# Optimization experiments

Measured on AMD Instinct MI355X. Metric: run time of the kernel, lower is better.

The kernel has to match this reference:

```python
import jax, jax.numpy as jnp
import numpy as np

N_EMB = 512
E_DIM = 64
COMMIT_COST = 0.25


def setup_inputs() -> dict:
    key = jax.random.key(0)
    k1, k2 = jax.random.split(key)
    z = jax.random.normal(k1, (32, E_DIM, 64, 64), dtype=jnp.float32)  # [B,C,H,W], C==e_dim
    # nn.Embedding weight init: uniform(-1/n_emb, 1/n_emb)
    emb_weight = jax.random.uniform(k2, (N_EMB, E_DIM), dtype=jnp.float32,
                                    minval=-1.0 / N_EMB, maxval=1.0 / N_EMB)
    return {"z": z, "emb_weight": emb_weight}


def reference(z, emb_weight):
    sg = jax.lax.stop_gradient
    B, C, H, W = z.shape
    zp = jnp.transpose(z, (0, 2, 3, 1))            # [B,H,W,C]
    zf = zp.reshape(-1, C)                          # [N,C]
    # pairwise squared distances: ||z||^2 + ||e||^2 - 2 z e^T  -> [N, n_emb]
    d = (jnp.sum(zf * zf, axis=1, keepdims=True)
         + jnp.sum(emb_weight * emb_weight, axis=1)
         - 2.0 * jnp.matmul(zf, emb_weight.T))
    idx = jnp.argmin(d, axis=1)                     # [N]
    min_encodings = jax.nn.one_hot(idx, N_EMB, dtype=z.dtype)  # [N, n_emb]
    # one-hot @ weight == direct gather
    z_q = jnp.take(emb_weight, idx, axis=0).reshape(zp.shape)  # [B,H,W,C]
    loss = (jnp.mean((sg(z_q) - zp) ** 2)
            + COMMIT_COST * jnp.mean((z_q - sg(zp)) ** 2))
    z_q = zp + sg(z_q - zp)                         # straight-through
    e_mean = jnp.mean(min_encodings, axis=0)
    perplexity = jnp.exp(-jnp.sum(e_mean * jnp.log(e_mean + 1e-10)))
    z_q = jnp.transpose(z_q, (0, 3, 1, 2))          # back to [B,C,H,W]
    return (loss, z_q, perplexity, min_encodings, idx[:, None])
```

## Files before the change

### kernel.cpp

```cpp
#include <hip/hip_runtime.h>
#include <math.h>

#define OUT_ZQ   1LL
#define OUT_PERP 8388609LL
#define OUT_ENC  8388610LL
#define OUT_IDX  75497474LL

#define WS_HIST   0
#define WS_LOSS64 512
#define WS_ESUM   1024
#define WS_PK     4096
#define LOSS_SCALE 16777216.0

typedef __attribute__((ext_vector_type(8))) short bf16x8;
typedef __attribute__((ext_vector_type(4))) float f32x4;

__device__ __forceinline__ unsigned short f2bf(float f) {
  unsigned u = __builtin_bit_cast(unsigned, f);
  u += 0x7FFFu + ((u >> 16) & 1u);
  return (unsigned short)(u >> 16);
}

__global__ void vq_prep(const float* __restrict__ E, float* __restrict__ ws) {
#pragma clang fp contract(off)
  const int T   = blockIdx.x;
  const int tid = threadIdx.x;
  const int l   = tid & 63;
  const int kk  = tid >> 6;
  const int g = l >> 4, ln16 = l & 15;
  {
    const float* ej = E + (size_t)(T * 16 + ln16) * 64;
    const int c0 = kk * 32 + 4 * g;
    bf16x8 v;
#pragma unroll
    for (int i = 0; i < 4; ++i) v[i]     = (short)f2bf(ej[c0 + i]);
#pragma unroll
    for (int i = 0; i < 4; ++i) v[4 + i] = (short)f2bf(ej[c0 + 16 + i]);
    ((bf16x8*)(ws + WS_PK))[(T * 2 + kk) * 64 + l] = v;
  }
  if (tid < 16) {
    const int j = T * 16 + tid;
    const float* e = E + (size_t)j * 64;
    float q0=e[0]*e[0],q1=e[1]*e[1],q2=e[2]*e[2],q3=e[3]*e[3];
    float q4=e[4]*e[4],q5=e[5]*e[5],q6=e[6]*e[6],q7=e[7]*e[7];
#pragma unroll
    for (int i = 8; i < 64; i += 8) {
      q0+=e[i+0]*e[i+0]; q1+=e[i+1]*e[i+1]; q2+=e[i+2]*e[i+2]; q3+=e[i+3]*e[i+3];
      q4+=e[i+4]*e[i+4]; q5+=e[i+5]*e[i+5]; q6+=e[i+6]*e[i+6]; q7+=e[i+7]*e[i+7];
    }
    ws[WS_ESUM + j] = ((q0+q1)+(q2+q3))+((q4+q5)+(q6+q7));
  }
  if (T == 0) {
#pragma unroll
    for (int k = 0; k < 4; ++k) ((int*)ws)[WS_HIST + tid + k * 128] = 0;
    if (tid == 0) *((unsigned long long*)(ws + WS_LOSS64)) = 0ull;
  }
}

__global__ __launch_bounds__(256, 4) void vq_main(const float* __restrict__ z,
                                                  const float* __restrict__ E,
                                                  float* __restrict__ ws,
                                                  float* __restrict__ out) {
#pragma clang fp contract(off)
  const int tid  = threadIdx.x;
  const int lane = tid & 63;
  const int wv   = __builtin_amdgcn_readfirstlane(tid >> 6);
  const int g    = lane >> 4;
  const int ln16 = lane & 15;
  const int row  = blockIdx.x;
  const int b = row >> 6, h = row & 63;
  const size_t zbase = (size_t)b * 262144 + (size_t)h * 64;
  const float* __restrict__ esg = ws + WS_ESUM;
  const bf16x8* __restrict__ pkt = (const bf16x8*)(ws + WS_PK);
  float4* __restrict__ enc4 = (float4*)(out + OUT_ENC + (size_t)row * 32768);
  const float4 zz4 = {0.f, 0.f, 0.f, 0.f};
#define FILLC(cc) _Pragma("unroll") \
  for (int fi = (cc)*8; fi < (cc)*8 + 8; ++fi) enc4[(size_t)fi * 256 + tid] = zz4;

  __shared__ float lds_z[64][65];
  __shared__ float s_zsum[64];
  __shared__ float s_qpart[4][64];
  __shared__ float s_qthr[64];
  __shared__ int   s_cnt[64];
  __shared__ int   s_ovf[64];
  __shared__ int   s_idx[64];
  __shared__ int   s_cand[64][12];
  __shared__ float s_dcand[64][12];
  __shared__ float s_l[4];

#pragma unroll
  for (int k = 0; k < 16; ++k) {
    int c = k * 4 + wv;
    lds_z[lane][c] = z[zbase + (size_t)c * 4096 + lane];
  }
  if (tid < 64) { s_cnt[tid] = 0; s_ovf[tid] = 0; }
  FILLC(0)
  __syncthreads();

  if (tid < 64) {
    const float* zl = &lds_z[tid][0];
    float q0=zl[0]*zl[0],q1=zl[1]*zl[1],q2=zl[2]*zl[2],q3=zl[3]*zl[3];
    float q4=zl[4]*zl[4],q5=zl[5]*zl[5],q6=zl[6]*zl[6],q7=zl[7]*zl[7];
#pragma unroll
    for (int i = 8; i < 64; i += 8) {
      q0+=zl[i+0]*zl[i+0]; q1+=zl[i+1]*zl[i+1]; q2+=zl[i+2]*zl[i+2]; q3+=zl[i+3]*zl[i+3];
      q4+=zl[i+4]*zl[i+4]; q5+=zl[i+5]*zl[i+5]; q6+=zl[i+6]*zl[i+6]; q7+=zl[i+7]*zl[i+7];
    }
    s_zsum[tid] = ((q0+q1)+(q2+q3))+((q4+q5)+(q6+q7));
  }

  bf16x8 Af[4][2];
#pragma unroll
  for (int mt = 0; mt < 4; ++mt) {
    int m = mt * 16 + ln16;
#pragma unroll
    for (int kk = 0; kk < 2; ++kk) {
      int c0 = kk * 32 + 4 * g;
      bf16x8 v;
#pragma unroll
      for (int i = 0; i < 4; ++i) v[i]     = (short)f2bf(lds_z[m][c0 + i]);
#pragma unroll
      for (int i = 0; i < 4; ++i) v[4 + i] = (short)f2bf(lds_z[m][c0 + 16 + i]);
      Af[mt][kk] = v;
    }
  }

  float qmin[4][4];
#pragma unroll
  for (int mt = 0; mt < 4; ++mt)
#pragma unroll
    for (int r = 0; r < 4; ++r) qmin[mt][r] = 1e30f;
#pragma unroll
  for (int t = 0; t < 8; ++t) {
    const int T = wv * 8 + t;
    const int j = T * 16 + ln16;
    bf16x8 B0 = pkt[(T * 2 + 0) * 64 + lane];
    bf16x8 B1 = pkt[(T * 2 + 1) * 64 + lane];
    float es = esg[j];
#pragma unroll
    for (int mt = 0; mt < 4; ++mt) {
      f32x4 C = {0.f, 0.f, 0.f, 0.f};
      C = __builtin_amdgcn_mfma_f32_16x16x32_bf16(Af[mt][0], B0, C, 0, 0, 0);
      C = __builtin_amdgcn_mfma_f32_16x16x32_bf16(Af[mt][1], B1, C, 0, 0, 0);
#pragma unroll
      for (int r = 0; r < 4; ++r)
        qmin[mt][r] = fminf(qmin[mt][r], es - 2.0f * C[r]);
    }
  }
#pragma unroll
  for (int off = 1; off < 16; off <<= 1)
#pragma unroll
    for (int mt = 0; mt < 4; ++mt)
#pragma unroll
      for (int r = 0; r < 4; ++r)
        qmin[mt][r] = fminf(qmin[mt][r], __shfl_xor(qmin[mt][r], off));
  if (ln16 == 0)
#pragma unroll
    for (int mt = 0; mt < 4; ++mt)
#pragma unroll
      for (int r = 0; r < 4; ++r)
        s_qpart[wv][mt * 16 + g * 4 + r] = qmin[mt][r];
  FILLC(1)
  __syncthreads();
  if (tid < 64) {
    float qm = fminf(fminf(s_qpart[0][tid], s_qpart[1][tid]),
                     fminf(s_qpart[2][tid], s_qpart[3][tid]));
    s_qthr[tid] = qm + (2.5e-4f * sqrtf(s_zsum[tid]) + 1e-4f);
  }
  __syncthreads();

#pragma unroll
  for (int t = 0; t < 8; ++t) {
    const int T = wv * 8 + t;
    const int j = T * 16 + ln16;
    bf16x8 B0 = pkt[(T * 2 + 0) * 64 + lane];
    bf16x8 B1 = pkt[(T * 2 + 1) * 64 + lane];
    float es = esg[j];
#pragma unroll
    for (int mt = 0; mt < 4; ++mt) {
      f32x4 C = {0.f, 0.f, 0.f, 0.f};
      C = __builtin_amdgcn_mfma_f32_16x16x32_bf16(Af[mt][0], B0, C, 0, 0, 0);
      C = __builtin_amdgcn_mfma_f32_16x16x32_bf16(Af[mt][1], B1, C, 0, 0, 0);
#pragma unroll
      for (int r = 0; r < 4; ++r) {
        float q = es - 2.0f * C[r];
        int m = mt * 16 + g * 4 + r;
        if (q <= s_qthr[m]) {
          int pos = atomicAdd(&s_cnt[m], 1);
          if (pos < 12) s_cand[m][pos] = j; else s_ovf[m] = 1;
        }
      }
    }
  }
  FILLC(2)
  __syncthreads();

  {
    const int m = tid & 63;
    const float* zl = &lds_z[m][0];
    int cnt = s_cnt[m]; if (cnt > 12) cnt = 12;
    for (int s = wv; s < cnt; s += 4) {
      int j = s_cand[m][s];
      const float* ej = E + (size_t)j * 64;
      float a = 0.f;
#pragma unroll
      for (int c = 0; c < 64; ++c) a = fmaf(zl[c], ej[c], a);
      s_dcand[m][s] = (s_zsum[m] + esg[j]) - 2.0f * a;
    }
  }
  FILLC(3)
  __syncthreads();

  if (tid < 64) {
    const int m = tid;
    int cnt = s_cnt[m];
    int bi;
    if (cnt == 0 || cnt > 12 || s_ovf[m]) {
      const float* zl = &lds_z[m][0];
      float bd = 1e30f; bi = 0;
      for (int j = 0; j < 512; ++j) {
        const float* ej = E + (size_t)j * 64;
        float a = 0.f;
        for (int c = 0; c < 64; ++c) a = fmaf(zl[c], ej[c], a);
        float d = (s_zsum[m] + esg[j]) - 2.0f * a;
        if (d < bd) { bd = d; bi = j; }
      }
    } else {
      float bd = 1e30f; bi = 1 << 30;
      for (int s = 0; s < cnt; ++s) {
        float d = s_dcand[m][s]; int j = s_cand[m][s];
        if (d < bd || (d == bd && j < bi)) { bd = d; bi = j; }
      }
    }
    s_idx[m] = bi;
    out[OUT_IDX + (size_t)row * 64 + m] = (float)bi;
    atomicAdd(&((int*)ws)[WS_HIST + bi], 1);
  }
  __syncthreads();

  {
    float lsum = 0.f;
    const int p = s_idx[lane];
    const float* Ep = E + (size_t)p * 64;
#pragma unroll
    for (int k = 0; k < 16; ++k) {
      int c = wv * 16 + k;
      float ev = Ep[c];
      float d = ev - lds_z[lane][c];
      lsum = fmaf(d, d, lsum);
      out[OUT_ZQ + zbase + (size_t)c * 4096 + lane] = ev;
    }
    for (int off = 32; off; off >>= 1) lsum += __shfl_down(lsum, off);
    if (lane == 0) s_l[wv] = lsum;
  }
  __syncthreads();

  if (tid < 64)
    out[OUT_ENC + (size_t)row * 32768 + (size_t)tid * 512 + s_idx[tid]] = 1.0f;
  if (tid == 0) {
    float bl = (s_l[0] + s_l[1]) + (s_l[2] + s_l[3]);
    unsigned long long fx = (unsigned long long)((double)bl * LOSS_SCALE);
    atomicAdd((unsigned long long*)(ws + WS_LOSS64), fx);
  }
#undef FILLC
}

__global__ void vq_final(const float* __restrict__ ws, float* __restrict__ out) {
  int j = threadIdx.x;
  const int* hist = (const int*)ws + WS_HIST;
  float p = (float)hist[j] * (1.f / 131072.f);
  float t = -p * logf(p + 1e-10f);
  for (int off = 32; off; off >>= 1) t += __shfl_down(t, off);
  __shared__ float st[8];
  int wv = j >> 6, ln = j & 63;
  if (ln == 0) st[wv] = t;
  __syncthreads();
  if (j == 0) {
    float e = 0.f;
#pragma unroll
    for (int i = 0; i < 8; ++i) e += st[i];
    out[OUT_PERP] = expf(e);
    double ls = (double)*((const unsigned long long*)(ws + WS_LOSS64)) * (1.0 / LOSS_SCALE);
    out[0] = (float)(ls * (1.25 / 8388608.0));
  }
}

extern "C" void kernel_launch(void* const* d_in, const int* in_sizes, int n_in,
                              void* d_out, int out_size, void* d_ws, size_t ws_size,
                              hipStream_t stream) {
  const float* z = (const float*)d_in[0];
  const float* E = (const float*)d_in[1];
  float* out = (float*)d_out;
  float* ws  = (float*)d_ws;
  vq_prep<<<32, 128, 0, stream>>>(E, ws);
  vq_main<<<2048, 256, 0, stream>>>(z, E, ws, out);
  vq_final<<<1, 512, 0, stream>>>(ws, out);
}
```

Baseline: 114.0 us.

## Fuse final reduction into main kernel via last-block ticket; raise MFMA wave priority

New measurement: 228.8 us. +100.7%, slower.

```diff
diff --git a/kernel.cpp b/kernel.cpp
--- a/kernel.cpp
+++ b/kernel.cpp
@@ -8,6 +8,7 @@
 
 #define WS_HIST   0
 #define WS_LOSS64 512
+#define WS_TICKET 516
 #define WS_ESUM   1024
 #define WS_PK     4096
 #define LOSS_SCALE 16777216.0
@@ -53,7 +54,10 @@
   if (T == 0) {
 #pragma unroll
     for (int k = 0; k < 4; ++k) ((int*)ws)[WS_HIST + tid + k * 128] = 0;
-    if (tid == 0) *((unsigned long long*)(ws + WS_LOSS64)) = 0ull;
+    if (tid == 0) {
+      *((unsigned long long*)(ws + WS_LOSS64)) = 0ull;
+      ((int*)ws)[WS_TICKET] = 0;
+    }
   }
 }
 
@@ -87,6 +91,7 @@
   __shared__ int   s_cand[64][12];
   __shared__ float s_dcand[64][12];
   __shared__ float s_l[4];
+  __shared__ int   s_ticket;
 
 #pragma unroll
   for (int k = 0; k < 16; ++k) {
@@ -130,6 +135,7 @@
   for (int mt = 0; mt < 4; ++mt)
 #pragma unroll
     for (int r = 0; r < 4; ++r) qmin[mt][r] = 1e30f;
+  __builtin_amdgcn_s_setprio(1);
 #pragma unroll
   for (int t = 0; t < 8; ++t) {
     const int T = wv * 8 + t;
@@ -147,6 +153,7 @@
         qmin[mt][r] = fminf(qmin[mt][r], es - 2.0f * C[r]);
     }
   }
+  __builtin_amdgcn_s_setprio(0);
 #pragma unroll
   for (int off = 1; off < 16; off <<= 1)
 #pragma unroll
@@ -169,6 +176,7 @@
   }
   __syncthreads();
 
+  __builtin_amdgcn_s_setprio(1);
 #pragma unroll
   for (int t = 0; t < 8; ++t) {
     const int T = wv * 8 + t;
@@ -192,6 +200,7 @@
       }
     }
   }
+  __builtin_amdgcn_s_setprio(0);
   FILLC(2)
   __syncthreads();
 
@@ -261,28 +270,31 @@
     float bl = (s_l[0] + s_l[1]) + (s_l[2] + s_l[3]);
     unsigned long long fx = (unsigned long long)((double)bl * LOSS_SCALE);
     atomicAdd((unsigned long long*)(ws + WS_LOSS64), fx);
+    asm volatile("s_waitcnt vmcnt(0)" ::: "memory");
+    __threadfence();
+    s_ticket = atomicAdd(&((int*)ws)[WS_TICKET], 1);
+  }
+  __syncthreads();
+
+  if (s_ticket == 2047 && wv == 0) {
+    float t = 0.f;
+#pragma unroll
+    for (int k = 0; k < 8; ++k) {
+      int j = lane * 8 + k;
+      int cnt = atomicAdd(&((int*)ws)[WS_HIST + j], 0);
+      float p = (float)cnt * (1.f / 131072.f);
+      t += -p * logf(p + 1e-10f);
+    }
+    for (int off = 32; off; off >>= 1) t += __shfl_down(t, off);
+    if (lane == 0) {
+      out[OUT_PERP] = expf(t);
+      unsigned long long ls64 =
+          atomicAdd((unsigned long long*)(ws + WS_LOSS64), 0ull);
+      double ls = (double)ls64 * (1.0 / LOSS_SCALE);
+      out[0] = (float)(ls * (1.25 / 8388608.0));
+    }
   }
 #undef FILLC
-}
-
-__global__ void vq_final(const float* __restrict__ ws, float* __restrict__ out) {
-  int j = threadIdx.x;
-  const int* hist = (const int*)ws + WS_HIST;
-  float p = (float)hist[j] * (1.f / 131072.f);
-  float t = -p * logf(p + 1e-10f);
-  for (int off = 32; off; off >>= 1) t += __shfl_down(t, off);
-  __shared__ float st[8];
-  int wv = j >> 6, ln = j & 63;
-  if (ln == 0) st[wv] = t;
-  __syncthreads();
-  if (j == 0) {
-    float e = 0.f;
-#pragma unroll
-    for (int i = 0; i < 8; ++i) e += st[i];
-    out[OUT_PERP] = expf(e);
-    double ls = (double)*((const unsigned long long*)(ws + WS_LOSS64)) * (1.0 / LOSS_SCALE);
-    out[0] = (float)(ls * (1.25 / 8388608.0));
-  }
 }
 
 extern "C" void kernel_launch(void* const* d_in, const int* in_sizes, int n_in,
@@ -294,5 +306,4 @@
   float* ws  = (float*)d_ws;
   vq_prep<<<32, 128, 0, stream>>>(E, ws);
   vq_main<<<2048, 256, 0, stream>>>(z, E, ws, out);
-  vq_final<<<1, 512, 0, stream>>>(ws, out);
 }
```
